# Optimization experiments

Measured on AMD Instinct MI355X. Metric: run time of the kernel, lower is better.

The kernel has to match this reference:

```python
import jax, jax.numpy as jnp
import numpy as np

B, T, C, H = 4, 2048, 1024, 16
HD = C // H


def setup_inputs() -> dict:
    key = jax.random.key(0)
    k1, k2, k3, k4 = jax.random.split(key, 4)
    x = jax.random.normal(k1, (B, T, C), dtype=jnp.float32)
    pad_mask = jnp.ones((B, T), dtype=jnp.int32)
    # Linear weights stored as (in, out); torch Linear uses W.T so math is identical.
    w_attn = jax.random.normal(k2, (C, 3 * C), dtype=jnp.float32) * (1.0 / np.sqrt(C))
    w_proj = jax.random.normal(k3, (C, C), dtype=jnp.float32) * (1.0 / np.sqrt(C))
    b_proj = jax.random.normal(k4, (C,), dtype=jnp.float32) * 0.01
    return {"x": x, "pad_mask": pad_mask, "w_attn": w_attn, "w_proj": w_proj, "b_proj": b_proj}


def reference(x, pad_mask, w_attn, w_proj, b_proj):
    Bx, Tx, Cx = x.shape
    hd = Cx // H
    qkv = x @ w_attn                                  # (B,T,3C)
    q, k, v = jnp.split(qkv, 3, axis=2)
    # (B,T,C) -> (B,H,T,hd)
    q = q.reshape(Bx, Tx, H, hd).transpose(0, 2, 1, 3)
    k = k.reshape(Bx, Tx, H, hd).transpose(0, 2, 1, 3)
    v = v.reshape(Bx, Tx, H, hd).transpose(0, 2, 1, 3)
    att = jnp.einsum('bhqd,bhkd->bhqk', q, k) * (1.0 / np.sqrt(hd))
    causal = jnp.tril(jnp.ones((Tx, Tx), dtype=bool))[None, None]       # (1,1,T,T)
    keep = causal & (pad_mask[:, None, None, :] != 0)                   # (B,1,T,T) broadcast
    att = jnp.where(keep, att, -jnp.inf)
    att = jax.nn.softmax(att, axis=-1)
    # dropout p=0.0 (eval) -> identity
    y = jnp.einsum('bhqk,bhkd->bhqd', att, v)
    y = y.transpose(0, 2, 1, 3).reshape(Bx, Tx, Cx)
    return y @ w_proj + b_proj
```

## Files before the change

kernel.cpp:

```cpp
#include <hip/hip_runtime.h>
#include <hip/hip_bf16.h>


using short8  = __attribute__((ext_vector_type(8))) short;
using short4_ = __attribute__((ext_vector_type(4))) short;
using float4_ = __attribute__((ext_vector_type(4))) float;

#define Bb   4
#define Tt   2048
#define Cc   1024
#define Hh   16
#define HDd  64

__device__ __forceinline__ float bf2f(unsigned short u) {
    union { float f; unsigned int i; } x; x.i = ((unsigned int)u) << 16; return x.f;
}
__device__ __forceinline__ unsigned short f2bf(float f) {
    union { float f; unsigned int i; } x; x.f = f;
    unsigned int r = x.i + 0x7fff + ((x.i >> 16) & 1);
    return (unsigned short)(r >> 16);
}
__device__ __forceinline__ float4_ bmfma(short8 a, short8 b, float4_ c) {
    return __builtin_amdgcn_mfma_f32_16x16x32_bf16(a, b, c, 0, 0, 0);
}
__device__ __forceinline__ float ex2(float x) {
    return __builtin_amdgcn_exp2f(x);
}
__device__ __forceinline__ void gl2lds16(const unsigned short* g, unsigned short* l) {
    __builtin_amdgcn_global_load_lds(
        (const __attribute__((address_space(1))) void*)g,
        (__attribute__((address_space(3))) void*)l, 16, 0, 0);
}

__global__ __launch_bounds__(256) void convert_f32_bf16(
    const float* __restrict__ in, unsigned short* __restrict__ out)
{
    size_t idx = ((size_t)blockIdx.x * 256 + threadIdx.x) * 8;
    float4_ f0 = *(const float4_*)&in[idx];
    float4_ f1 = *(const float4_*)&in[idx + 4];
    short8 h;
    h[0] = (short)f2bf(f0[0]); h[1] = (short)f2bf(f0[1]);
    h[2] = (short)f2bf(f0[2]); h[3] = (short)f2bf(f0[3]);
    h[4] = (short)f2bf(f1[0]); h[5] = (short)f2bf(f1[1]);
    h[6] = (short)f2bf(f1[2]); h[7] = (short)f2bf(f1[3]);
    *(short8*)&out[idx] = h;
}

__global__ __launch_bounds__(256) void transpose_f32_bf16(
    const float* __restrict__ in, unsigned short* __restrict__ out,
    int R, int Ccols)
{
    __shared__ unsigned short tile[32][33];
    int c0 = blockIdx.x * 32, r0 = blockIdx.y * 32;
    int tx = threadIdx.x & 31, ty = threadIdx.x >> 5;
    for (int o = 0; o < 32; o += 8)
        tile[ty + o][tx] = f2bf(in[(size_t)(r0 + ty + o) * Ccols + c0 + tx]);
    __syncthreads();
    for (int o = 0; o < 32; o += 8)
        out[(size_t)(c0 + ty + o) * R + r0 + tx] = tile[tx][ty + o];
}

#define GBK 64

__device__ __forceinline__ void gemm128_main(
    const unsigned short* __restrict__ A, const unsigned short* __restrict__ Bt,
    int K, int m0, int n0,
    unsigned short* As, unsigned short* Bs, float4_ acc[4][4], bool swapT)
{
    int tid  = threadIdx.x;
    int wave = tid >> 6, lane = tid & 63;
    int wm = (wave >> 1) * 64, wn = (wave & 1) * 64;
    int lr = lane & 15, lg = lane >> 4;
    int srow = tid >> 3;
    int scol = (tid & 7) * 8;

    for (int k0 = 0; k0 < K; k0 += GBK) {
        #pragma unroll
        for (int j = 0; j < 4; j++) {
            int row = j * 32 + srow;
            gl2lds16(&A [(size_t)(m0 + row) * K + k0 + scol], &As[row * GBK + scol]);
            gl2lds16(&Bt[(size_t)(n0 + row) * K + k0 + scol], &Bs[row * GBK + scol]);
        }
        __syncthreads();
        #pragma unroll
        for (int ks = 0; ks < GBK; ks += 32) {
            short8 af[4], bf[4];
            #pragma unroll
            for (int i = 0; i < 4; i++) {
                af[i] = *(const short8*)&As[(wm + i * 16 + lr) * GBK + ks + lg * 8];
                bf[i] = *(const short8*)&Bs[(wn + i * 16 + lr) * GBK + ks + lg * 8];
            }
            if (!swapT) {
                #pragma unroll
                for (int i = 0; i < 4; i++)
                    #pragma unroll
                    for (int j = 0; j < 4; j++)
                        acc[i][j] = bmfma(af[i], bf[j], acc[i][j]);
            } else {
                #pragma unroll
                for (int i = 0; i < 4; i++)
                    #pragma unroll
                    for (int j = 0; j < 4; j++)
                        acc[i][j] = bmfma(bf[i], af[j], acc[i][j]);
            }
        }
        __syncthreads();
    }
}

__device__ __forceinline__ void supertile_remap(int& m0, int& n0)
{
    int bx = blockIdx.x, by = blockIdx.y;
    int mt = ((by & 7) << 3) | (bx & 7);
    int nt = ((by >> 3) << 3) | (bx >> 3);
    m0 = mt * 128; n0 = nt * 128;
}

__global__ __launch_bounds__(256) void gemm_qkv(
    const unsigned short* __restrict__ A,
    const unsigned short* __restrict__ Bt,
    unsigned short* __restrict__ Q,
    unsigned short* __restrict__ Ko,
    unsigned short* __restrict__ V)
{
    __shared__ unsigned short As[128 * GBK];
    __shared__ unsigned short Bs[128 * GBK];
    int m0, n0;
    supertile_remap(m0, n0);
    bool vblk = (n0 >= 2048);
    float4_ acc[4][4] = {};
    gemm128_main(A, Bt, 1024, m0, n0, As, Bs, acc, vblk);

    int lane = threadIdx.x & 63, wave = threadIdx.x >> 6;
    int wm = (wave >> 1) * 64, wn = (wave & 1) * 64;
    int lr = lane & 15, lg = lane >> 4;
    if (!vblk) {
        #pragma unroll
        for (int i = 0; i < 4; i++)
            #pragma unroll
            for (int j = 0; j < 4; j++) {
                int n = n0 + wn + 16 * j + lr;
                int which = n >> 10;
                int c = n & 1023;
                int h = c >> 6, d = c & 63;
                unsigned short* dst = (which == 0) ? Q : Ko;
                float sc2 = (which == 0) ? 0.1803368801f : 1.0f;
                #pragma unroll
                for (int r = 0; r < 4; r++) {
                    int m = m0 + wm + 16 * i + lg * 4 + r;
                    int b = m >> 11, t = m & 2047;
                    dst[(((size_t)(b * Hh + h) * Tt) + t) * HDd + d] = f2bf(acc[i][j][r] * sc2);
                }
            }
    } else {
        #pragma unroll
        for (int i = 0; i < 4; i++)
            #pragma unroll
            for (int j = 0; j < 4; j++) {
                int m = m0 + wm + 16 * j + lr;
                int b = m >> 11, t = m & 2047;
                #pragma unroll
                for (int r = 0; r < 4; r++) {
                    int n = n0 + wn + 16 * i + lg * 4 + r;
                    int c = n - 2048;
                    int h = c >> 6, d = c & 63;
                    V[(((size_t)(b * Hh + h) * HDd) + d) * Tt + t] = f2bf(acc[i][j][r]);
                }
            }
    }
}

__global__ __launch_bounds__(256) void gemm_proj(
    const unsigned short* __restrict__ A,
    const unsigned short* __restrict__ Bt,
    const float* __restrict__ bias,
    float* __restrict__ Out)
{
    __shared__ unsigned short As[128 * GBK];
    __shared__ unsigned short Bs[128 * GBK];
    int m0, n0;
    supertile_remap(m0, n0);
    float4_ acc[4][4] = {};
    gemm128_main(A, Bt, 1024, m0, n0, As, Bs, acc, false);

    int lane = threadIdx.x & 63, wave = threadIdx.x >> 6;
    int wm = (wave >> 1) * 64, wn = (wave & 1) * 64;
    int lr = lane & 15, lg = lane >> 4;
    #pragma unroll
    for (int i = 0; i < 4; i++)
        #pragma unroll
        for (int j = 0; j < 4; j++) {
            int n = n0 + wn + 16 * j + lr;
            float bv = bias[n];
            #pragma unroll
            for (int r = 0; r < 4; r++) {
                int m = m0 + wm + 16 * i + lg * 4 + r;
                Out[(size_t)m * 1024 + n] = acc[i][j][r] + bv;
            }
        }
}

#define DPAD 72

__global__ __launch_bounds__(256) void attn_fwd(
    const unsigned short* __restrict__ Q,
    const unsigned short* __restrict__ Kg,
    const unsigned short* __restrict__ Vg,
    const int* __restrict__ pad,
    unsigned short* __restrict__ Y)
{
    __shared__ unsigned short smem[128 * DPAD];
    unsigned short* Kt = smem;
    unsigned short* Vt = smem + 64 * DPAD;

    int flat = blockIdx.x;
    int qb = 31 - (flat >> 6);
    int bh = flat & 63;
    int b  = bh >> 4, h = bh & 15;
    const size_t base = (size_t)bh * Tt * HDd;
    int tid  = threadIdx.x;
    int wave = tid >> 6, lane = tid & 63;
    int lr = lane & 15, lg = lane >> 4;
    int q0 = qb * 64 + wave * 16;
    unsigned short* Pw = &Kt[wave * 16 * DPAD];
    const int* padRow = pad + b * Tt;

    int r8 = tid >> 3;
    int c8 = (tid & 7) * 8;

    short8 qf0 = *(const short8*)&Q[base + (size_t)(q0 + lr) * HDd + lg * 8];
    short8 qf1 = *(const short8*)&Q[base + (size_t)(q0 + lr) * HDd + 32 + lg * 8];

    float m_i = -1e30f, l_i = 0.f;
    float4_ o_acc[4];
    #pragma unroll
    for (int dt = 0; dt < 4; dt++) o_acc[dt] = (float4_){0.f, 0.f, 0.f, 0.f};

    int ebase = (lg & 1) * 4;
    int hnib  = lg >> 1;
    int q2    = (2 * lr) & 7;

    for (int kt = 0; kt <= qb; kt++) {
        int k0 = kt * 64;
        {
            short8 ka = *(const short8*)&Kg[base + (size_t)(k0 + r8) * HDd + c8];
            short8 kb = *(const short8*)&Kg[base + (size_t)(k0 + r8 + 32) * HDd + c8];
            short8 va = *(const short8*)&Vg[base + (size_t)r8 * Tt + k0 + c8];
            short8 vb = *(const short8*)&Vg[base + (size_t)(r8 + 32) * Tt + k0 + c8];
            *(short8*)&Kt[r8 * DPAD + c8]        = ka;
            *(short8*)&Kt[(r8 + 32) * DPAD + c8] = kb;
            *(short8*)&Vt[r8 * DPAD + c8]        = va;
            *(short8*)&Vt[(r8 + 32) * DPAD + c8] = vb;
        }
        int pvld = padRow[k0 + lane];
        unsigned long long pm = __ballot(pvld != 0);
        __syncthreads();

        float4_ s[4];
        #pragma unroll
        for (int nt = 0; nt < 4; nt++) {
            short8 kf0 = *(const short8*)&Kt[(nt * 16 + lr) * DPAD + lg * 8];
            short8 kf1 = *(const short8*)&Kt[(nt * 16 + lr) * DPAD + 32 + lg * 8];
            float4_ a = (float4_){0.f, 0.f, 0.f, 0.f};
            a = bmfma(kf0, qf0, a);
            a = bmfma(kf1, qf1, a);
            s[nt] = a;
        }
        if (kt == qb) {
            #pragma unroll
            for (int nt = 0; nt < 4; nt++)
                #pragma unroll
                for (int r = 0; r < 4; r++) {
                    int kl = nt * 16 + lg * 4 + r;
                    bool kpv = (pm >> kl) & 1ull;
                    if (!kpv || kl > wave * 16 + lr) s[nt][r] = -1e30f;
                }
        } else if (pm != ~0ull) {
            #pragma unroll
            for (int nt = 0; nt < 4; nt++)
                #pragma unroll
                for (int r = 0; r < 4; r++) {
                    int kl = nt * 16 + lg * 4 + r;
                    bool kpv = (pm >> kl) & 1ull;
                    s[nt][r] = kpv ? s[nt][r] : -1e30f;
                }
        }
        float v = fmaxf(fmaxf(s[0][0], s[0][1]), fmaxf(s[0][2], s[0][3]));
        #pragma unroll
        for (int nt = 1; nt < 4; nt++)
            v = fmaxf(v, fmaxf(fmaxf(s[nt][0], s[nt][1]), fmaxf(s[nt][2], s[nt][3])));
        v = fmaxf(v, __shfl_xor(v, 16, 64));
        v = fmaxf(v, __shfl_xor(v, 32, 64));
        float m_new = fmaxf(m_i, v);
        float alpha = ex2(m_i - m_new);
        float rsum = 0.f;
        #pragma unroll
        for (int nt = 0; nt < 4; nt++)
            #pragma unroll
            for (int r = 0; r < 4; r++) {
                float p = ex2(s[nt][r] - m_new);
                s[nt][r] = p;
                rsum += p;
            }
        rsum += __shfl_xor(rsum, 16, 64);
        rsum += __shfl_xor(rsum, 32, 64);
        l_i = l_i * alpha + rsum;
        m_i = m_new;

        #pragma unroll
        for (int r = 0; r < 4; r++) {
            float ar = __shfl(alpha, (lg << 2) + r, 64);
            #pragma unroll
            for (int dt = 0; dt < 4; dt++)
                o_acc[dt][r] *= ar;
        }

        __syncthreads();

        #pragma unroll
        for (int nt = 0; nt < 4; nt++) {
            short4_ w;
            w[0] = (short)f2bf(s[nt][0]); w[1] = (short)f2bf(s[nt][1]);
            w[2] = (short)f2bf(s[nt][2]); w[3] = (short)f2bf(s[nt][3]);
            int p = (2 * nt + hnib - q2) & 7;
            *(short4_*)&Pw[lr * DPAD + p * 8 + ebase] = w;
        }
        short8 pf0 = *(const short8*)&Pw[lr * DPAD + (((lg - q2) & 7) << 3)];
        short8 pf1 = *(const short8*)&Pw[lr * DPAD + (((4 + lg - q2) & 7) << 3)];
        #pragma unroll
        for (int dt = 0; dt < 4; dt++) {
            int d = dt * 16 + lr;
            short8 vf0 = *(const short8*)&Vt[d * DPAD + lg * 8];
            short8 vf1 = *(const short8*)&Vt[d * DPAD + 32 + lg * 8];
            o_acc[dt] = bmfma(pf0, vf0, o_acc[dt]);
            o_acc[dt] = bmfma(pf1, vf1, o_acc[dt]);
        }
        __syncthreads();
    }

    #pragma unroll
    for (int r = 0; r < 4; r++) {
        float lr_ = __shfl(l_i, (lg << 2) + r, 64);
        int qrow = q0 + lg * 4 + r;
        #pragma unroll
        for (int dt = 0; dt < 4; dt++)
            Y[((size_t)b * Tt + qrow) * Cc + h * HDd + dt * 16 + lr] =
                f2bf(o_acc[dt][r] / lr_);
    }
}

extern "C" void kernel_launch(void* const* d_in, const int* in_sizes, int n_in,
                              void* d_out, int out_size, void* d_ws, size_t ws_size,
                              hipStream_t stream)
{
    const float* x      = (const float*)d_in[0];
    const int*   pad    = (const int*)d_in[1];
    const float* w_attn = (const float*)d_in[2];
    const float* w_proj = (const float*)d_in[3];
    const float* b_proj = (const float*)d_in[4];
    float*       out    = (float*)d_out;

    unsigned short* Wta = (unsigned short*)d_ws;
    unsigned short* Wtp = Wta + (size_t)3072 * 1024;
    unsigned short* Xb  = Wtp + (size_t)1024 * 1024;
    unsigned short* Yb  = Xb;
    unsigned short* Qb  = Xb + (size_t)8192 * 1024;
    unsigned short* Kb  = Qb + (size_t)Bb * Hh * Tt * HDd;
    unsigned short* Vb  = Kb + (size_t)Bb * Hh * Tt * HDd;

    convert_f32_bf16<<<dim3(4096), 256, 0, stream>>>(x, Xb);
    transpose_f32_bf16<<<dim3(3072 / 32, 1024 / 32), 256, 0, stream>>>(w_attn, Wta, 1024, 3072);
    transpose_f32_bf16<<<dim3(1024 / 32, 1024 / 32), 256, 0, stream>>>(w_proj, Wtp, 1024, 1024);
    gemm_qkv<<<dim3(8192 / 128, 3072 / 128), 256, 0, stream>>>(Xb, Wta, Qb, Kb, Vb);
    attn_fwd<<<dim3(2048), 256, 0, stream>>>(Qb, Kb, Vb, pad, Yb);
    gemm_proj<<<dim3(8192 / 128, 1024 / 128), 256, 0, stream>>>(Yb, Wtp, b_proj, out);
}
```

Baseline: 283.7 us.

## Prefetch next K/V tile into registers and double-buffer shared memory in attention

The attention loop now loads the next K/V tile and pad mask from global memory into registers while the current tile is being computed, and alternates between two shared-memory buffers. This removes the trailing barrier per iteration and hides global load latency behind the MFMA work. In exchange, shared memory doubles and register pressure rises from the held prefetch values, which could lower occupancy.

After: 284.3 us. No clear change (+0.2%).

```diff
diff --git a/kernel.cpp b/kernel.cpp
--- a/kernel.cpp
+++ b/kernel.cpp
@@ -209,9 +209,7 @@
     const int* __restrict__ pad,
     unsigned short* __restrict__ Y)
 {
-    __shared__ unsigned short smem[128 * DPAD];
-    unsigned short* Kt = smem;
-    unsigned short* Vt = smem + 64 * DPAD;
+    __shared__ unsigned short smem[4 * 64 * DPAD];
 
     int flat = blockIdx.x;
     int qb = 31 - (flat >> 6);
@@ -222,7 +220,6 @@
     int wave = tid >> 6, lane = tid & 63;
     int lr = lane & 15, lg = lane >> 4;
     int q0 = qb * 64 + wave * 16;
-    unsigned short* Pw = &Kt[wave * 16 * DPAD];
     const int* padRow = pad + b * Tt;
 
     int r8 = tid >> 3;
@@ -240,21 +237,31 @@
     int hnib  = lg >> 1;
     int q2    = (2 * lr) & 7;
 
+    short8 kr0 = *(const short8*)&Kg[base + (size_t)r8 * HDd + c8];
+    short8 kr1 = *(const short8*)&Kg[base + (size_t)(r8 + 32) * HDd + c8];
+    short8 vr0 = *(const short8*)&Vg[base + (size_t)r8 * Tt + c8];
+    short8 vr1 = *(const short8*)&Vg[base + (size_t)(r8 + 32) * Tt + c8];
+    int pvld = padRow[lane];
+
     for (int kt = 0; kt <= qb; kt++) {
-        int k0 = kt * 64;
-        {
-            short8 ka = *(const short8*)&Kg[base + (size_t)(k0 + r8) * HDd + c8];
-            short8 kb = *(const short8*)&Kg[base + (size_t)(k0 + r8 + 32) * HDd + c8];
-            short8 va = *(const short8*)&Vg[base + (size_t)r8 * Tt + k0 + c8];
-            short8 vb = *(const short8*)&Vg[base + (size_t)(r8 + 32) * Tt + k0 + c8];
-            *(short8*)&Kt[r8 * DPAD + c8]        = ka;
-            *(short8*)&Kt[(r8 + 32) * DPAD + c8] = kb;
-            *(short8*)&Vt[r8 * DPAD + c8]        = va;
-            *(short8*)&Vt[(r8 + 32) * DPAD + c8] = vb;
-        }
-        int pvld = padRow[k0 + lane];
+        int cur = kt & 1;
+        unsigned short* Kt = smem + cur * (2 * 64 * DPAD);
+        unsigned short* Vt = Kt + 64 * DPAD;
+        *(short8*)&Kt[r8 * DPAD + c8]        = kr0;
+        *(short8*)&Kt[(r8 + 32) * DPAD + c8] = kr1;
+        *(short8*)&Vt[r8 * DPAD + c8]        = vr0;
+        *(short8*)&Vt[(r8 + 32) * DPAD + c8] = vr1;
         unsigned long long pm = __ballot(pvld != 0);
         __syncthreads();
+
+        if (kt < qb) {
+            int k1 = kt * 64 + 64;
+            kr0 = *(const short8*)&Kg[base + (size_t)(k1 + r8) * HDd + c8];
+            kr1 = *(const short8*)&Kg[base + (size_t)(k1 + r8 + 32) * HDd + c8];
+            vr0 = *(const short8*)&Vg[base + (size_t)r8 * Tt + k1 + c8];
+            vr1 = *(const short8*)&Vg[base + (size_t)(r8 + 32) * Tt + k1 + c8];
+            pvld = padRow[k1 + lane];
+        }
 
         float4_ s[4];
         #pragma unroll
@@ -317,6 +324,7 @@
 
         __syncthreads();
 
+        unsigned short* Pw = &Kt[wave * 16 * DPAD];
         #pragma unroll
         for (int nt = 0; nt < 4; nt++) {
             short4_ w;
@@ -335,7 +343,6 @@
             o_acc[dt] = bmfma(pf0, vf0, o_acc[dt]);
             o_acc[dt] = bmfma(pf1, vf1, o_acc[dt]);
         }
-        __syncthreads();
     }
 
     #pragma unroll
```
